# Performance work log

Measured on AMD Instinct MI355X. Metric: run time of the kernel, lower is better.

## Reference

```python
import jax, jax.numpy as jnp
import numpy as np

B, T, DIM = 2, 2048, 1040
H = 16
HD = (DIM - 1) // H  # 64 spatial dims per head; per-head width = HD + 1
EPS = 1e-6


def _rotary_tables(seq_len, dtype):
    inv_freq = 1.0 / (10000.0 ** (jnp.arange(0, HD, 2, dtype=jnp.float32) / (HD - 2 * EPS)))
    t = jnp.arange(seq_len, dtype=jnp.float32)
    freqs = jnp.outer(t, inv_freq)  # [T, HD//2]
    cos = jnp.cos(freqs).astype(dtype)[None, :, None, :]  # [1,T,1,HD//2]
    sin = jnp.sin(freqs).astype(dtype)[None, :, None, :]
    return cos, sin


def _apply_hyp_rotary(x, cos, sin):
    # x: [B,T,H,HD+1]; component 0 is the Lorentz time coordinate
    x_sp = x[..., 1:]
    d = x_sp.shape[-1] // 2
    x1, x2 = x_sp[..., :d], x_sp[..., d:]
    y1 = x1 * cos + x2 * sin
    y2 = -x1 * sin + x2 * cos
    rot = jnp.clip(jnp.concatenate([y1, y2], axis=-1), -1000.0, 1000.0)
    sp_sq = jnp.clip(jnp.sum(rot * rot, axis=-1, keepdims=True), 0.0, 1e6)
    new_x0 = jnp.sqrt(1.0 + sp_sq + EPS)  # re-project onto hyperboloid
    return jnp.concatenate([new_x0, rot], axis=-1)


def setup_inputs() -> dict:
    key = jax.random.key(0)
    kx, kq, kk, kv, kp = jax.random.split(key, 5)
    scale = 0.02  # xavier_normal gain 0.02 in the original
    x = jax.random.normal(kx, (B, T, DIM), dtype=jnp.float32)
    Wq = jax.random.normal(kq, (DIM, DIM), dtype=jnp.float32) * scale
    Wk = jax.random.normal(kk, (DIM, DIM), dtype=jnp.float32) * scale
    Wv = jax.random.normal(kv, (DIM, DIM), dtype=jnp.float32) * scale
    Wp = jax.random.normal(kp, (DIM, DIM), dtype=jnp.float32) * scale
    return {"x": x, "Wq": Wq, "Wk": Wk, "Wv": Wv, "Wp": Wp}


def reference(x, Wq, Wk, Wv, Wp):
    b, t, _ = x.shape
    q = (x @ Wq.T).reshape(b, t, H, HD + 1)
    k = (x @ Wk.T).reshape(b, t, H, HD + 1)
    v = (x @ Wv.T).reshape(b, t, H, HD + 1)
    cos, sin = _rotary_tables(t, x.dtype)
    q = _apply_hyp_rotary(q, cos, sin)
    k = _apply_hyp_rotary(k, cos, sin)
    # Lorentzian inner product scores: -q0*k0 + <q_sp, k_sp>
    spatial = jnp.einsum('bthd,bshd->bhts', q[..., 1:], k[..., 1:])
    lorentz = jnp.einsum('bth,bsh->bhts', q[..., 0], k[..., 0])
    logits = jnp.clip((spatial - lorentz) / (HD ** 0.5), -100.0, 100.0)
    attn = jax.nn.softmax(logits, axis=-1)
    y = jnp.einsum('bhts,bshd->bthd', attn, v).reshape(b, t, DIM)
    return y @ Wp.T
```

## Files before the change

kernel.cpp:

```cpp
#include <hip/hip_runtime.h>
#include <math.h>

#define B_   2
#define T_   2048
#define DIM_ 1040
#define H_   16
#define HD_  64
#define HD1_ 65
#define NELEM (B_*T_*DIM_)

#define KP_   1056
#define NP_   1152
#define NP3_  3456
#define SEGS_ 132
#define MROWS_ (B_*T_)

#define NBH_  (B_*H_)
#define VTR_  72

#define PR_A_ (NP3_*SEGS_)
#define PR_B_ (PR_A_ + MROWS_*SEGS_)
#define PR_C_ (PR_B_ + NBH_*7*256)
#define PR_D_ (PR_C_ + NP_*SEGS_)

typedef __attribute__((ext_vector_type(8))) __bf16 bf16x8;
typedef __attribute__((ext_vector_type(4))) float f32x4;
typedef __attribute__((ext_vector_type(8))) unsigned short ushort8;

static __device__ __forceinline__ unsigned pack_bf16(float lo, float hi) {
    __bf16 a = (__bf16)lo, c = (__bf16)hi;
    unsigned short ua, uc;
    __builtin_memcpy(&ua, &a, 2);
    __builtin_memcpy(&uc, &c, 2);
    return ((unsigned)uc << 16) | ua;
}

static __device__ __forceinline__ float exp2_fast(float x) {
    float r;
    asm("v_exp_f32 %0, %1" : "=v"(r) : "v"(x));
    return r;
}

static __device__ __forceinline__ void conv_row_plain(
    const float* __restrict__ in, __bf16* __restrict__ out, int r, int s,
    int rows_in)
{
    float v[8];
    if (r < rows_in && s < 130) {
        const float4 f0 = *(const float4*)(in + (size_t)r * DIM_ + s * 8);
        const float4 f1 = *(const float4*)(in + (size_t)r * DIM_ + s * 8 + 4);
        v[0]=f0.x; v[1]=f0.y; v[2]=f0.z; v[3]=f0.w;
        v[4]=f1.x; v[5]=f1.y; v[6]=f1.z; v[7]=f1.w;
    } else {
        #pragma unroll
        for (int i = 0; i < 8; ++i) v[i] = 0.0f;
    }
    __bf16 t[8] __attribute__((aligned(16)));
    #pragma unroll
    for (int i = 0; i < 8; ++i) t[i] = (__bf16)v[i];
    *(ushort8*)(out) = *(const ushort8*)(t);
}

__global__ __launch_bounds__(256)
void prep_all(const float* __restrict__ x,  const float* __restrict__ Wq,
              const float* __restrict__ Wk, const float* __restrict__ Wv,
              const float* __restrict__ Wp, __bf16* __restrict__ xb,
              __bf16* __restrict__ Wb3, __bf16* __restrict__ VT,
              __bf16* __restrict__ WpB)
{
    const int gid = blockIdx.x * 256 + threadIdx.x;
    if (gid < PR_A_) {
        const int r = gid / SEGS_, s = gid - r * SEGS_;
        const int seg = r / NP_, rr = r - seg * NP_;
        const float* in = (seg == 0) ? Wq : (seg == 1) ? Wk : Wv;
        conv_row_plain(in, Wb3 + (size_t)r * KP_ + s * 8, rr, s, DIM_);
    } else if (gid < PR_B_) {
        const int g = gid - PR_A_;
        const int r = g / SEGS_, s = g - r * SEGS_;
        conv_row_plain(x, xb + (size_t)r * KP_ + s * 8, r, s, MROWS_);
    } else if (gid < PR_C_) {
        const int cid = gid - PR_B_;
        const int bh  = cid / 1792;
        const int rem = cid - bh * 1792;
        const int row = 65 + rem / 256;
        const int tc  = rem - (row - 65) * 256;
        const unsigned val = (row == 65) ? 0x3F803F80u : 0u;
        unsigned* p = (unsigned*)(VT + ((size_t)bh * VTR_ + row) * T_ + tc * 8);
        p[0] = val; p[1] = val; p[2] = val; p[3] = val;
    } else {
        const int g = gid - PR_C_;
        const int r = g / SEGS_, s = g - r * SEGS_;
        conv_row_plain(Wp, WpB + (size_t)r * KP_ + s * 8, r, s, DIM_);
    }
}

__device__ __forceinline__ void gload_lds16(const void* g, void* l) {
    __builtin_amdgcn_global_load_lds(
        (const __attribute__((address_space(1))) void*)g,
        (__attribute__((address_space(3))) void*)l, 16, 0, 0);
}

#define GEMM_PURE_CORE(Ac_, Bw_, N0_, M0_)                                    \
    __shared__ __bf16 As[128 * 96];                                           \
    __shared__ __bf16 Bs[128 * 96];                                           \
    const int tid  = threadIdx.x;                                             \
    const int lane = tid & 63;                                                \
    const int w    = tid >> 6;                                                \
    const int wr   = (w >> 1) * 64, wc = (w & 1) * 64;                        \
    const __bf16* gap[6]; const __bf16* gb[6];                                \
    _Pragma("unroll")                                                         \
    for (int qi = 0; qi < 6; ++qi) {                                          \
        const int cid = qi * 256 + tid;                                       \
        const int rr  = cid / 12, cc = cid - rr * 12;                         \
        gap[qi] = Ac_ + (size_t)(M0_ + rr) * KP_ + cc * 8;                    \
        gb[qi]  = Bw_ + (size_t)(N0_ + rr) * KP_ + cc * 8;                    \
    }                                                                         \
    f32x4 acc[4][4];                                                          \
    _Pragma("unroll")                                                         \
    for (int i = 0; i < 4; ++i)                                               \
        _Pragma("unroll")                                                     \
        for (int j = 0; j < 4; ++j) acc[i][j] = (f32x4){0.f, 0.f, 0.f, 0.f};  \
    const __bf16* pa = As + (wr + (lane & 15)) * 96 + (lane >> 4) * 8;        \
    const __bf16* pb = Bs + (wc + (lane & 15)) * 96 + (lane >> 4) * 8;        \
    for (int k0 = 0; k0 < KP_; k0 += 96) {                                    \
        __syncthreads();                                                      \
        _Pragma("unroll")                                                     \
        for (int qi = 0; qi < 6; ++qi) {                                      \
            gload_lds16(gap[qi] + k0, As + (qi * 256 + tid) * 8);             \
            gload_lds16(gb[qi]  + k0, Bs + (qi * 256 + tid) * 8);             \
        }                                                                     \
        __syncthreads();                                                      \
        _Pragma("unroll")                                                     \
        for (int ks = 0; ks < 3; ++ks) {                                      \
            bf16x8 a[4], b[4];                                                \
            _Pragma("unroll")                                                 \
            for (int i = 0; i < 4; ++i)                                       \
                a[i] = *(const bf16x8*)(pa + i * 16 * 96 + ks * 32);          \
            _Pragma("unroll")                                                 \
            for (int j = 0; j < 4; ++j)                                       \
                b[j] = *(const bf16x8*)(pb + j * 16 * 96 + ks * 32);          \
            __builtin_amdgcn_s_setprio(1);                                    \
            _Pragma("unroll")                                                 \
            for (int i = 0; i < 4; ++i)                                       \
                _Pragma("unroll")                                             \
                for (int j = 0; j < 4; ++j)                                   \
                    acc[i][j] = __builtin_amdgcn_mfma_f32_16x16x32_bf16(      \
                        a[i], b[j], acc[i][j], 0, 0, 0);                      \
            __builtin_amdgcn_s_setprio(0);                                    \
        }                                                                     \
    }

__global__ __launch_bounds__(256)
void gemm_qkv_b(const __bf16* __restrict__ Ac, const __bf16* __restrict__ Bw,
                float* __restrict__ Cq, float* __restrict__ Ck,
                __bf16* __restrict__ VTout)
{
    const int bid = blockIdx.x;
    const int gid = (bid & 7) * 108 + (bid >> 3);
    const int n0  = (gid >> 5) * 128;
    const int m0  = (gid & 31) * 128;
    GEMM_PURE_CORE(Ac, Bw, n0, m0)

    const int seg = n0 / NP_;
    const int rbase = m0 + wr + (lane >> 4) * 4;
    const int cbase = n0 - seg * NP_ + wc + (lane & 15);

    if (seg < 2) {
        float* C = seg ? Ck : Cq;
        #pragma unroll
        for (int i = 0; i < 4; ++i)
            #pragma unroll
            for (int j = 0; j < 4; ++j) {
                const int n = cbase + j * 16;
                if (n < DIM_) {
                    #pragma unroll
                    for (int r = 0; r < 4; ++r)
                        C[(size_t)(rbase + i * 16 + r) * DIM_ + n] = acc[i][j][r];
                }
            }
    } else {
        #pragma unroll
        for (int i = 0; i < 4; ++i) {
            const int tg = rbase + i * 16;
            const int bb = tg >> 11, tt = tg & (T_ - 1);
            #pragma unroll
            for (int j = 0; j < 4; ++j) {
                const int n = cbase + j * 16;
                if (n < DIM_) {
                    const int h = n / 65, d = n - h * 65;
                    const size_t off =
                        ((size_t)(bb * H_ + h) * VTR_ + d) * T_ + tt;
                    uint2 pk;
                    pk.x = pack_bf16(acc[i][j][0], acc[i][j][1]);
                    pk.y = pack_bf16(acc[i][j][2], acc[i][j][3]);
                    *(uint2*)(VTout + off) = pk;
                }
            }
        }
    }
}

__global__ __launch_bounds__(256)
void gemm_out_b(const __bf16* __restrict__ Ac, const __bf16* __restrict__ Bw,
                float* __restrict__ C)
{
    const int bid = blockIdx.x;
    const int gid = (bid & 7) * 36 + (bid >> 3);
    const int n0  = (gid >> 5) * 128;
    const int m0  = (gid & 31) * 128;
    GEMM_PURE_CORE(Ac, Bw, n0, m0)

    const int rbase = m0 + wr + (lane >> 4) * 4;
    const int cbase = n0 + wc + (lane & 15);
    #pragma unroll
    for (int i = 0; i < 4; ++i)
        #pragma unroll
        for (int j = 0; j < 4; ++j) {
            const int n = cbase + j * 16;
            if (n < DIM_) {
                #pragma unroll
                for (int r = 0; r < 4; ++r)
                    C[(size_t)(rbase + i * 16 + r) * DIM_ + n] = acc[i][j][r];
            }
        }
}

__global__ __launch_bounds__(256)
void rotary2(const float* __restrict__ Xq, const float* __restrict__ Xk,
             __bf16* __restrict__ QB, __bf16* __restrict__ KB,
             float* __restrict__ Q0, float* __restrict__ K0)
{
    const int gwid = (blockIdx.x * 256 + threadIdx.x) >> 6;
    const int lane = threadIdx.x & 63;
    const int which = gwid >> 16;
    const int wid   = gwid & 65535;

    const int h  = wid & (H_ - 1);
    const int bt = wid >> 4;
    const int t  = bt & (T_ - 1);
    const int b  = bt >> 11;
    const float* base = (which ? Xk : Xq) + (size_t)bt * DIM_ + h * HD1_;

    const int j = lane & 31;
    const float pw = powf(10000.0f, (float)j * (1.0f / 32.0f));
    const float fr = (float)t * (1.0f / pw);
    const float cs = cosf(fr);
    const float sn = sinf(fr);

    const float x1 = base[1 + j];
    const float x2 = base[33 + j];

    float rot = (lane < 32) ? (x1 * cs + x2 * sn)
                            : (x2 * cs - x1 * sn);
    rot = fminf(fmaxf(rot, -1000.0f), 1000.0f);

    float sq = rot * rot;
    #pragma unroll
    for (int off = 32; off >= 1; off >>= 1)
        sq += __shfl_xor(sq, off, 64);
    sq = fminf(fmaxf(sq, 0.0f), 1.0e6f);

    const float x0 = sqrtf((1.0f + sq) + 1.0e-6f);

    const size_t bht = (size_t)(b * H_ + h) * T_ + t;
    (which ? KB : QB)[bht * 64 + lane] = (__bf16)rot;
    if (lane == 0) (which ? K0 : Q0)[bht] = x0;
}

__global__ __launch_bounds__(256)
void attn_mfma6(const __bf16* __restrict__ QB, const __bf16* __restrict__ KB,
                const __bf16* __restrict__ VT, const float* __restrict__ Q0,
                const float* __restrict__ K0, __bf16* __restrict__ yb)
{
    __shared__ __bf16 Qt[64 * 64] __attribute__((aligned(16)));
    __shared__ __bf16 Kt[2][64 * 64] __attribute__((aligned(16)));
    __shared__ __bf16 Vt[80 * 64] __attribute__((aligned(16)));
    __shared__ __bf16 Pt[64 * 72] __attribute__((aligned(16)));

    const int tid  = threadIdx.x;
    const int lane = tid & 63;
    const int w    = tid >> 6;
    const int lx   = lane & 15;
    const int ly   = lane >> 4;
    const int bh   = blockIdx.x;
    const int q0r  = blockIdx.y * 64;

    const float SCALE = 0.18033688f;

    const __bf16* QBb = QB + (size_t)bh * T_ * 64;
    const __bf16* KBb = KB + (size_t)bh * T_ * 64;
    const __bf16* VTb = VT + (size_t)bh * VTR_ * T_;
    const float*  Q0b = Q0 + (size_t)bh * T_;
    const float*  K0b = K0 + (size_t)bh * T_;

    #pragma unroll
    for (int qi = 0; qi < 2; ++qi) {
        const int cid = qi * 256 + tid;
        const int r = cid >> 3, j = cid & 7;
        gload_lds16(QBb + (size_t)(q0r + r) * 64 + (j ^ (r & 7)) * 8,
                    Qt + cid * 8);
    }
    ((unsigned*)Vt)[2304 + tid] = 0u;

    float q0v[4];
    #pragma unroll
    for (int r = 0; r < 4; ++r)
        q0v[r] = Q0b[q0r + w * 16 + ly * 4 + r];

    int offk[2], offv[3];
    #pragma unroll
    for (int qi = 0; qi < 2; ++qi) {
        const int cid = qi * 256 + tid;
        const int r = cid >> 3, j = cid & 7;
        offk[qi] = r * 64 + (j ^ (r & 7)) * 8;
    }
    #pragma unroll
    for (int qi = 0; qi < 3; ++qi) {
        const int cid = qi * 256 + tid;
        const int d = cid >> 3, j = cid & 7;
        offv[qi] = d * T_ + (j ^ (d & 7)) * 8;
    }

    #pragma unroll
    for (int qi = 0; qi < 2; ++qi)
        gload_lds16(KBb + offk[qi], &Kt[0][(qi * 256 + tid) * 8]);

    float k0nxt[4];
    #pragma unroll
    for (int n = 0; n < 4; ++n) k0nxt[n] = K0b[n * 16 + lx];

    f32x4 acc_o[5];
    #pragma unroll
    for (int n = 0; n < 5; ++n) acc_o[n] = (f32x4){0.f, 0.f, 0.f, 0.f};

    int cur = 0;
    for (int it = 0; it < T_ / 64; ++it) {
        const int s0 = it * 64;
        __syncthreads();

        gload_lds16(VTb + s0 + offv[0], Vt + tid * 8);
        gload_lds16(VTb + s0 + offv[1], Vt + (256 + tid) * 8);
        if (tid < 64)
            gload_lds16(VTb + s0 + offv[2], Vt + (512 + tid) * 8);

        float k0S[4];
        #pragma unroll
        for (int n = 0; n < 4; ++n) k0S[n] = k0nxt[n] * SCALE;

        if (it + 1 < T_ / 64) {
            const int s1 = s0 + 64;
            #pragma unroll
            for (int qi = 0; qi < 2; ++qi)
                gload_lds16(KBb + (size_t)s1 * 64 + offk[qi],
                            &Kt[cur ^ 1][(qi * 256 + tid) * 8]);
            #pragma unroll
            for (int n = 0; n < 4; ++n) k0nxt[n] = K0b[s1 + n * 16 + lx];
        }

        bf16x8 aq[2];
        #pragma unroll
        for (int ks = 0; ks < 2; ++ks)
            aq[ks] = *(const bf16x8*)
                &Qt[(w * 16 + lx) * 64 + ((ks * 4 + ly) ^ (lx & 7)) * 8];

        f32x4 sc[4];
        __builtin_amdgcn_s_setprio(1);
        #pragma unroll
        for (int n = 0; n < 4; ++n) {
            f32x4 c = (f32x4){0.f, 0.f, 0.f, 0.f};
            #pragma unroll
            for (int ks = 0; ks < 2; ++ks) {
                const bf16x8 bk = *(const bf16x8*)
                    &Kt[cur][(n * 16 + lx) * 64 +
                             ((ks * 4 + ly) ^ (lx & 7)) * 8];
                c = __builtin_amdgcn_mfma_f32_16x16x32_bf16(
                    aq[ks], bk, c, 0, 0, 0);
            }
            sc[n] = c;
        }
        __builtin_amdgcn_s_setprio(0);

        #pragma unroll
        for (int n = 0; n < 4; ++n)
            #pragma unroll
            for (int r = 0; r < 4; ++r) {
                const float p =
                    exp2_fast(fmaf(sc[n][r], SCALE, -q0v[r] * k0S[n]));
                Pt[(w * 16 + ly * 4 + r) * 72 + n * 16 + lx] = (__bf16)p;
            }

        __syncthreads();

        bf16x8 ap[2];
        #pragma unroll
        for (int ks = 0; ks < 2; ++ks)
            ap[ks] = *(const bf16x8*)
                &Pt[(w * 16 + lx) * 72 + ks * 32 + ly * 8];
        __builtin_amdgcn_s_setprio(1);
        #pragma unroll
        for (int n = 0; n < 5; ++n) {
            f32x4 c = acc_o[n];
            #pragma unroll
            for (int ks = 0; ks < 2; ++ks) {
                const bf16x8 bv = *(const bf16x8*)
                    &Vt[(n * 16 + lx) * 64 + ((ks * 4 + ly) ^ (lx & 7)) * 8];
                c = __builtin_amdgcn_mfma_f32_16x16x32_bf16(
                    ap[ks], bv, c, 0, 0, 0);
            }
            acc_o[n] = c;
        }
        __builtin_amdgcn_s_setprio(0);
        cur ^= 1;
    }

    const int b = bh >> 4, h = bh & 15;
    #pragma unroll
    for (int r = 0; r < 4; ++r) {
        const float l = __shfl(acc_o[4][r], (lane & 48) + 1, 64);
        const float inv = 1.0f / l;
        const int qrow = q0r + w * 16 + ly * 4 + r;
        __bf16* yrow = yb + (size_t)(b * T_ + qrow) * KP_ + h * HD1_;
        #pragma unroll
        for (int n = 0; n < 4; ++n)
            yrow[n * 16 + lx] = (__bf16)(acc_o[n][r] * inv);
        if (lx == 0) yrow[64] = (__bf16)(acc_o[4][r] * inv);
    }
}

extern "C" void kernel_launch(void* const* d_in, const int* in_sizes, int n_in,
                              void* d_out, int out_size, void* d_ws, size_t ws_size,
                              hipStream_t stream)
{
    const float* x  = (const float*)d_in[0];
    const float* Wq = (const float*)d_in[1];
    const float* Wk = (const float*)d_in[2];
    const float* Wv = (const float*)d_in[3];
    const float* Wp = (const float*)d_in[4];

    float*  q   = (float*)d_ws;
    float*  k   = q + NELEM;
    __bf16* xb  = (__bf16*)(k + NELEM);
    __bf16* Wb3 = xb + (size_t)MROWS_ * KP_;
    __bf16* QB  = Wb3 + (size_t)NP3_ * KP_;
    __bf16* KB  = QB + (size_t)NBH_ * T_ * 64;
    float*  q0f = (float*)(KB + (size_t)NBH_ * T_ * 64);
    float*  k0f = q0f + NBH_ * T_;
    __bf16* VT  = (__bf16*)(k0f + NBH_ * T_);
    __bf16* WpB = VT + (size_t)NBH_ * VTR_ * T_;
    __bf16* yb  = xb;

    float* out = (float*)d_out;

    dim3 blk(256);

    prep_all<<<dim3(PR_D_ / 256), blk, 0, stream>>>(
        x, Wq, Wk, Wv, Wp, xb, Wb3, VT, WpB);
    gemm_qkv_b<<<dim3(864), blk, 0, stream>>>(xb, Wb3, q, k, VT);

    rotary2<<<dim3(2 * (B_ * T_ * H_) / 4), blk, 0, stream>>>(
        q, k, QB, KB, q0f, k0f);

    attn_mfma6<<<dim3(NBH_, T_ / 64), blk, 0, stream>>>(
        QB, KB, VT, q0f, k0f, yb);

    gemm_out_b<<<dim3(288), blk, 0, stream>>>(yb, WpB, out);
}
```

Measured before the change: 228.7 us.

## Fold Lorentz time term and scale into augmented bf16 Q/K dot product

The rotary kernel now writes Q and K rows padded to 96 bf16 values. Q is pre-scaled, and extra columns encode the Lorentz time-coordinate product as a split-bf16 decomposition around a 5.25 offset. The attention kernel then gets the full logit from a third MFMA k-step and applies exp2 directly, with no per-element fma and no q0/k0 scalar loads. Q fragments are loaded straight from global memory into registers instead of going through LDS, and K tiles use a new swizzled 96-wide layout. In exchange each tile does 50% more QK MFMA work and moves more K bytes, and the bf16 splitting of x0 adds precision risk.

```diff
diff --git a/kernel.cpp b/kernel.cpp
--- a/kernel.cpp
+++ b/kernel.cpp
@@ -17,6 +17,7 @@
 
 #define NBH_  (B_*H_)
 #define VTR_  72
+#define QKW_  96
 
 #define PR_A_ (NP3_*SEGS_)
 #define PR_B_ (PR_A_ + MROWS_*SEGS_)
@@ -227,13 +228,14 @@
 
 __global__ __launch_bounds__(256)
 void rotary2(const float* __restrict__ Xq, const float* __restrict__ Xk,
-             __bf16* __restrict__ QB, __bf16* __restrict__ KB,
-             float* __restrict__ Q0, float* __restrict__ K0)
+             __bf16* __restrict__ QB, __bf16* __restrict__ KB)
 {
     const int gwid = (blockIdx.x * 256 + threadIdx.x) >> 6;
     const int lane = threadIdx.x & 63;
     const int which = gwid >> 16;
     const int wid   = gwid & 65535;
+
+    const float SCALE = 0.18033688f;
 
     const int h  = wid & (H_ - 1);
     const int bt = wid >> 4;
@@ -262,18 +264,30 @@
 
     const float x0 = sqrtf((1.0f + sq) + 1.0e-6f);
 
-    const size_t bht = (size_t)(b * H_ + h) * T_ + t;
-    (which ? KB : QB)[bht * 64 + lane] = (__bf16)rot;
-    if (lane == 0) (which ? K0 : Q0)[bht] = x0;
+    __bf16* XB = which ? KB : QB;
+    const size_t base96 = (size_t)((b * H_ + h) * T_ + t) * QKW_;
+    XB[base96 + lane] = which ? (__bf16)rot : (__bf16)(SCALE * rot);
+
+    if (lane < 32) {
+        float v = 0.0f;
+        const float d0 = x0 - 5.25f;
+        if (which) {
+            const float bh = (float)(__bf16)d0;
+            if (lane == 0 || lane == 2) v = bh;
+            else if (lane == 1) v = d0 - bh;
+        } else {
+            if (lane < 2) v = -SCALE * 5.25f;
+            else if (lane == 2) v = -SCALE * (float)(__bf16)d0;
+        }
+        XB[base96 + 64 + lane] = (__bf16)v;
+    }
 }
 
 __global__ __launch_bounds__(256)
-void attn_mfma6(const __bf16* __restrict__ QB, const __bf16* __restrict__ KB,
-                const __bf16* __restrict__ VT, const float* __restrict__ Q0,
-                const float* __restrict__ K0, __bf16* __restrict__ yb)
-{
-    __shared__ __bf16 Qt[64 * 64] __attribute__((aligned(16)));
-    __shared__ __bf16 Kt[2][64 * 64] __attribute__((aligned(16)));
+void attn_mfma7(const __bf16* __restrict__ QB, const __bf16* __restrict__ KB,
+                const __bf16* __restrict__ VT, __bf16* __restrict__ yb)
+{
+    __shared__ __bf16 Kt[2][64 * 96] __attribute__((aligned(16)));
     __shared__ __bf16 Vt[80 * 64] __attribute__((aligned(16)));
     __shared__ __bf16 Pt[64 * 72] __attribute__((aligned(16)));
 
@@ -285,53 +299,43 @@
     const int bh   = blockIdx.x;
     const int q0r  = blockIdx.y * 64;
 
-    const float SCALE = 0.18033688f;
-
-    const __bf16* QBb = QB + (size_t)bh * T_ * 64;
-    const __bf16* KBb = KB + (size_t)bh * T_ * 64;
+    const __bf16* QBb = QB + (size_t)bh * T_ * QKW_;
+    const __bf16* KBb = KB + (size_t)bh * T_ * QKW_;
     const __bf16* VTb = VT + (size_t)bh * VTR_ * T_;
-    const float*  Q0b = Q0 + (size_t)bh * T_;
-    const float*  K0b = K0 + (size_t)bh * T_;
-
-    #pragma unroll
-    for (int qi = 0; qi < 2; ++qi) {
-        const int cid = qi * 256 + tid;
-        const int r = cid >> 3, j = cid & 7;
-        gload_lds16(QBb + (size_t)(q0r + r) * 64 + (j ^ (r & 7)) * 8,
-                    Qt + cid * 8);
-    }
+
+    bf16x8 aq[3];
+    #pragma unroll
+    for (int ks = 0; ks < 3; ++ks)
+        aq[ks] = *(const bf16x8*)
+            (QBb + (size_t)(q0r + w * 16 + lx) * QKW_ + ks * 32 + ly * 8);
+
     ((unsigned*)Vt)[2304 + tid] = 0u;
 
-    float q0v[4];
-    #pragma unroll
-    for (int r = 0; r < 4; ++r)
-        q0v[r] = Q0b[q0r + w * 16 + ly * 4 + r];
-
-    int offk[2], offv[3];
-    #pragma unroll
-    for (int qi = 0; qi < 2; ++qi) {
-        const int cid = qi * 256 + tid;
-        const int r = cid >> 3, j = cid & 7;
-        offk[qi] = r * 64 + (j ^ (r & 7)) * 8;
-    }
+    int offk[3];
     #pragma unroll
     for (int qi = 0; qi < 3; ++qi) {
         const int cid = qi * 256 + tid;
-        const int d = cid >> 3, j = cid & 7;
-        offv[qi] = d * T_ + (j ^ (d & 7)) * 8;
-    }
-
-    #pragma unroll
-    for (int qi = 0; qi < 2; ++qi)
+        const int s = cid / 12, p = cid - s * 12;
+        const int c = (p & 12) | ((p - (s >> 1)) & 3);
+        offk[qi] = s * QKW_ + c * 8;
+    }
+    int offv[3];
+    #pragma unroll
+    for (int qi = 0; qi < 3; ++qi) {
+        const int cid = qi * 256 + tid;
+        const int d = cid >> 3, jj = cid & 7;
+        offv[qi] = d * T_ + (jj ^ (d & 7)) * 8;
+    }
+
+    #pragma unroll
+    for (int qi = 0; qi < 3; ++qi)
         gload_lds16(KBb + offk[qi], &Kt[0][(qi * 256 + tid) * 8]);
 
-    float k0nxt[4];
-    #pragma unroll
-    for (int n = 0; n < 4; ++n) k0nxt[n] = K0b[n * 16 + lx];
-
     f32x4 acc_o[5];
     #pragma unroll
     for (int n = 0; n < 5; ++n) acc_o[n] = (f32x4){0.f, 0.f, 0.f, 0.f};
+
+    const int rr = (ly + (lx >> 1)) & 3;
 
     int cur = 0;
     for (int it = 0; it < T_ / 64; ++it) {
@@ -343,25 +347,13 @@
         if (tid < 64)
             gload_lds16(VTb + s0 + offv[2], Vt + (512 + tid) * 8);
 
-        float k0S[4];
-        #pragma unroll
-        for (int n = 0; n < 4; ++n) k0S[n] = k0nxt[n] * SCALE;
-
         if (it + 1 < T_ / 64) {
-            const int s1 = s0 + 64;
-            #pragma unroll
-            for (int qi = 0; qi < 2; ++qi)
-                gload_lds16(KBb + (size_t)s1 * 64 + offk[qi],
+            const int koff = (s0 + 64) * QKW_;
+            #pragma unroll
+            for (int qi = 0; qi < 3; ++qi)
+                gload_lds16(KBb + koff + offk[qi],
                             &Kt[cur ^ 1][(qi * 256 + tid) * 8]);
-            #pragma unroll
-            for (int n = 0; n < 4; ++n) k0nxt[n] = K0b[s1 + n * 16 + lx];
-        }
-
-        bf16x8 aq[2];
-        #pragma unroll
-        for (int ks = 0; ks < 2; ++ks)
-            aq[ks] = *(const bf16x8*)
-                &Qt[(w * 16 + lx) * 64 + ((ks * 4 + ly) ^ (lx & 7)) * 8];
+        }
 
         f32x4 sc[4];
         __builtin_amdgcn_s_setprio(1);
@@ -369,10 +361,9 @@
         for (int n = 0; n < 4; ++n) {
             f32x4 c = (f32x4){0.f, 0.f, 0.f, 0.f};
             #pragma unroll
-            for (int ks = 0; ks < 2; ++ks) {
+            for (int ks = 0; ks < 3; ++ks) {
                 const bf16x8 bk = *(const bf16x8*)
-                    &Kt[cur][(n * 16 + lx) * 64 +
-                             ((ks * 4 + ly) ^ (lx & 7)) * 8];
+                    &Kt[cur][(n * 16 + lx) * 96 + ks * 32 + rr * 8];
                 c = __builtin_amdgcn_mfma_f32_16x16x32_bf16(
                     aq[ks], bk, c, 0, 0, 0);
             }
@@ -383,11 +374,9 @@
         #pragma unroll
         for (int n = 0; n < 4; ++n)
             #pragma unroll
-            for (int r = 0; r < 4; ++r) {
-                const float p =
-                    exp2_fast(fmaf(sc[n][r], SCALE, -q0v[r] * k0S[n]));
-                Pt[(w * 16 + ly * 4 + r) * 72 + n * 16 + lx] = (__bf16)p;
-            }
+            for (int r = 0; r < 4; ++r)
+                Pt[(w * 16 + ly * 4 + r) * 72 + n * 16 + lx] =
+                    (__bf16)exp2_fast(sc[n][r]);
 
         __syncthreads();
 
@@ -442,10 +431,8 @@
     __bf16* xb  = (__bf16*)(k + NELEM);
     __bf16* Wb3 = xb + (size_t)MROWS_ * KP_;
     __bf16* QB  = Wb3 + (size_t)NP3_ * KP_;
-    __bf16* KB  = QB + (size_t)NBH_ * T_ * 64;
-    float*  q0f = (float*)(KB + (size_t)NBH_ * T_ * 64);
-    float*  k0f = q0f + NBH_ * T_;
-    __bf16* VT  = (__bf16*)(k0f + NBH_ * T_);
+    __bf16* KB  = QB + (size_t)NBH_ * T_ * QKW_;
+    __bf16* VT  = KB + (size_t)NBH_ * T_ * QKW_;
     __bf16* WpB = VT + (size_t)NBH_ * VTR_ * T_;
     __bf16* yb  = xb;
 
@@ -457,11 +444,9 @@
         x, Wq, Wk, Wv, Wp, xb, Wb3, VT, WpB);
     gemm_qkv_b<<<dim3(864), blk, 0, stream>>>(xb, Wb3, q, k, VT);
 
-    rotary2<<<dim3(2 * (B_ * T_ * H_) / 4), blk, 0, stream>>>(
-        q, k, QB, KB, q0f, k0f);
-
-    attn_mfma6<<<dim3(NBH_, T_ / 64), blk, 0, stream>>>(
-        QB, KB, VT, q0f, k0f, yb);
+    rotary2<<<dim3(2 * (B_ * T_ * H_) / 4), blk, 0, stream>>>(q, k, QB, KB);
+
+    attn_mfma7<<<dim3(NBH_, T_ / 64), blk, 0, stream>>>(QB, KB, VT, yb);
 
     gemm_out_b<<<dim3(288), blk, 0, stream>>>(yb, WpB, out);
 }
```

Result: no change. 230.3 us (+0.7%).
